# Optimization experiments

Hardware: AMD Instinct MI355X
Metric: run time of the kernel (lower is better)

## Reference

```python
import jax, jax.numpy as jnp
import numpy as np

P, V, D = 1024, 49408, 512


def setup_inputs() -> dict:
    key = jax.random.key(0)
    k1, k2 = jax.random.split(key)
    prompt_embs = jax.random.normal(k1, (P, D), dtype=jnp.float32)
    clip_embs = jax.random.normal(k2, (V, D), dtype=jnp.float32)
    return {"prompt_embs": prompt_embs, "clip_embs": clip_embs}


def reference(prompt_embs, clip_embs):
    # torch.cdist(p=2): Euclidean distance matrix [P, V].
    # ||a-b||^2 = ||a||^2 + ||b||^2 - 2 a.b ; sqrt is monotone so argmin of
    # the (clamped) squared distance matches argmin of the true distance.
    a2 = jnp.sum(prompt_embs * prompt_embs, axis=-1, keepdims=True)   # [P,1]
    b2 = jnp.sum(clip_embs * clip_embs, axis=-1)                      # [V]
    ab = jnp.einsum("pd,vd->pv", prompt_embs, clip_embs)              # [P,V]
    d2 = jnp.maximum(a2 + b2[None, :] - 2.0 * ab, 0.0)                # [P,V]
    prompt_ids = jnp.argmin(d2, axis=1)                               # [P]
    new_embs = clip_embs[prompt_ids]                                  # [P,D] gather
    return new_embs, prompt_ids
```

## Files before the change

### kernel.cpp

```cpp
#include <hip/hip_runtime.h>
#include <stdint.h>

#define NP 1024
#define NV 49408
#define ND 512
#define NTILE 48

typedef __attribute__((ext_vector_type(8))) __bf16 bf16x8;
typedef __attribute__((ext_vector_type(4))) float f32x4;
typedef __attribute__((ext_vector_type(4))) int i32x4;

__device__ inline unsigned long long pack_sv(float s, unsigned v) {
  unsigned u = __float_as_uint(s);
  u = (u & 0x80000000u) ? ~u : (u | 0x80000000u);
  return ((unsigned long long)u << 32) | (unsigned long long)v;
}

__global__ __launch_bounds__(256) void pack_a_k(const float* __restrict__ src,
                                                __bf16* __restrict__ dst) {
  int lane = threadIdx.x & 63;
  int row = blockIdx.x * 4 + (threadIdx.x >> 6);
  const float* r = src + (size_t)row * ND + lane * 8;
  float4 x0 = *(const float4*)r;
  float4 x1 = *(const float4*)(r + 4);
  float xs[8] = {x0.x, x0.y, x0.z, x0.w, x1.x, x1.y, x1.z, x1.w};
  bf16x8 hi, lo;
#pragma unroll
  for (int j = 0; j < 8; ++j) {
    float x = xs[j];
    __bf16 h = (__bf16)x;
    hi[j] = h;
    lo[j] = (__bf16)(x - (float)h);
  }
  const int mb = row >> 4, rr = row & 15;
  const int tHi = lane >> 2, g = lane & 3;
  size_t cHi = (((size_t)tHi * 64) + mb) * 64 + g * 16 + rr;
  size_t cLo = (((size_t)(tHi + 16) * 64) + mb) * 64 + g * 16 + rr;
  *(bf16x8*)(dst + cHi * 8) = hi;
  *(bf16x8*)(dst + cLo * 8) = lo;
}

__global__ __launch_bounds__(256) void pack_b_k(const float* __restrict__ src,
                                                __bf16* __restrict__ dst,
                                                float* __restrict__ sumsq) {
  int lane = threadIdx.x & 63;
  int row = blockIdx.x * 4 + (threadIdx.x >> 6);
  const float* r = src + (size_t)row * ND + lane * 8;
  float4 x0 = *(const float4*)r;
  float4 x1 = *(const float4*)(r + 4);
  float xs[8] = {x0.x, x0.y, x0.z, x0.w, x1.x, x1.y, x1.z, x1.w};
  bf16x8 hi, lo;
  float ss = 0.f;
#pragma unroll
  for (int j = 0; j < 8; ++j) {
    float x = xs[j];
    ss += x * x;
    __bf16 h = (__bf16)x;
    hi[j] = h;
    lo[j] = (__bf16)(x - (float)h);
  }
  __bf16* drow = dst + (size_t)row * 1024 + lane * 8;
  *(bf16x8*)drow = hi;
  *(bf16x8*)(drow + 512) = lo;
#pragma unroll
  for (int m = 1; m < 64; m <<= 1) ss += __shfl_xor(ss, m);
  if (lane == 0) sumsq[row] = ss;
}


__device__ __attribute__((always_inline)) static inline
void gll16(const char* src, char* dst) {
  __builtin_amdgcn_global_load_lds(
      (const __attribute__((address_space(1))) void*)src,
      (__attribute__((address_space(3))) void*)dst, 16, 0, 0);
}

__device__ __attribute__((always_inline)) static inline
bf16x8 lds_read(unsigned addr) {
  i32x4 d;
  asm volatile("ds_read_b128 %0, %1" : "=v"(d) : "v"(addr));
  return __builtin_bit_cast(bf16x8, d);
}

#define FENCE asm volatile("" ::: "memory")

template <int PH>
__device__ __attribute__((always_inline)) static inline
void phase_op(f32x4 (&acc)[4][4], bf16x8 (&aE)[4], bf16x8 (&aO)[4],
              const char* Ab, const int (&voffA)[4],
              const char* srcBt, char* stB, unsigned bRead, int p) {
  constexpr int R = PH % 3;
  constexpr int RS = (PH + 2) % 3;
  const int kA = ((p + 1) & 31) * 65536;
  const int t2 = p + 2;
  const int kB = (t2 & 15) * 64 + (t2 >= 32 ? 1024 : 0);
  bf16x8 (&aN)[4] = (PH % 2 == 0) ? aO : aE;
  bf16x8 (&aC)[4] = (PH % 2 == 0) ? aE : aO;
#pragma unroll
  for (int m = 0; m < 4; ++m)
    aN[m] = *(const bf16x8*)(Ab + voffA[m] + kA);
  gll16(srcBt + kB, stB + RS * 8192);
  gll16(srcBt + kB + 131072, stB + RS * 8192 + 4096);
  bf16x8 b[4];
#pragma unroll
  for (int n = 0; n < 4; ++n)
    b[n] = lds_read(bRead + R * 8192 + n * 1024);
  asm volatile("s_waitcnt vmcnt(6) lgkmcnt(0)" ::: "memory");
  __builtin_amdgcn_sched_barrier(0);
  __builtin_amdgcn_s_setprio(1);
#pragma unroll
  for (int m = 0; m < 4; ++m)
#pragma unroll
    for (int n = 0; n < 4; ++n)
      acc[m][n] = __builtin_amdgcn_mfma_f32_16x16x32_bf16(aC[m], b[n], acc[m][n], 0, 0, 0);
  __builtin_amdgcn_s_setprio(0);
  FENCE;
  __builtin_amdgcn_s_barrier();
  FENCE;
}

__global__ __launch_bounds__(256, 3) void gemm_argmin_k(const __bf16* __restrict__ A,
                                                        const __bf16* __restrict__ B,
                                                        const float* __restrict__ b2,
                                                        unsigned long long* __restrict__ best) {
  __shared__ __align__(16) char lds[24576];
  const int tid = threadIdx.x;
  const int lane = tid & 63;
  const int wid = tid >> 6;
  const int wm = wid >> 1;
  const int wn = wid & 1;

  const int d = blockIdx.x;
  const int o = (d & 7) * 386 + (d >> 3);
  const int bm = (o & 7) * 128;
  const int bn = (o >> 3) * 128;

  const int r = lane & 15, g = lane >> 4;
  const int rh = r >> 1;
  const unsigned lds0 =
      (unsigned)(uintptr_t)(const __attribute__((address_space(3))) char*)(const char*)lds;
  const unsigned bRead = lds0 + wn * 4096 + rh * 128 + (r & 1) * 64 + (((g + rh) & 3) << 4);

  const char* Ab = (const char*)A;
  int voffA[4];
#pragma unroll
  for (int m = 0; m < 4; ++m)
    voffA[m] = ((bm >> 4) + wm * 4 + m) * 1024 + lane * 16;

  const int srow = 2 * (tid >> 3) + ((tid >> 2) & 1);
  const int sc16 = ((tid & 3) - (tid >> 3)) & 3;
  const char* srcBt = (const char*)B + (size_t)(bn + srow) * 2048 + sc16 * 16;
  char* stB = (char*)lds + tid * 16;

  f32x4 acc[4][4] = {};
  bf16x8 aE[4], aO[4];

#pragma unroll
  for (int m = 0; m < 4; ++m)
    aE[m] = *(const bf16x8*)(Ab + voffA[m]);
  gll16(srcBt + 0, stB + 0);
  gll16(srcBt + 0 + 131072, stB + 4096);
  gll16(srcBt + 64, stB + 8192);
  gll16(srcBt + 64 + 131072, stB + 8192 + 4096);
  asm volatile("s_waitcnt vmcnt(2)" ::: "memory");
  FENCE;
  __builtin_amdgcn_s_barrier();
  FENCE;

#pragma unroll 1
  for (int it = 0; it < 8; ++it) {
    const int p0 = 6 * it;
    phase_op<0>(acc, aE, aO, Ab, voffA, srcBt, stB, bRead, p0 + 0);
    phase_op<1>(acc, aE, aO, Ab, voffA, srcBt, stB, bRead, p0 + 1);
    phase_op<2>(acc, aE, aO, Ab, voffA, srcBt, stB, bRead, p0 + 2);
    phase_op<3>(acc, aE, aO, Ab, voffA, srcBt, stB, bRead, p0 + 3);
    phase_op<4>(acc, aE, aO, Ab, voffA, srcBt, stB, bRead, p0 + 4);
    phase_op<5>(acc, aE, aO, Ab, voffA, srcBt, stB, bRead, p0 + 5);
  }

  float bb[4];
#pragma unroll
  for (int n = 0; n < 4; ++n) bb[n] = b2[bn + wn * 64 + n * 16 + r];
#pragma unroll
  for (int m = 0; m < 4; ++m) {
#pragma unroll
    for (int reg = 0; reg < 4; ++reg) {
      unsigned long long pk = ~0ull;
#pragma unroll
      for (int n = 0; n < 4; ++n) {
        float s = bb[n] - 2.0f * acc[m][n][reg];
        unsigned long long cand = pack_sv(s, (unsigned)(bn + wn * 64 + n * 16 + r));
        pk = (cand < pk) ? cand : pk;
      }
#pragma unroll
      for (int msk = 1; msk < 16; msk <<= 1) {
        unsigned long long o2 = __shfl_xor(pk, msk);
        pk = (o2 < pk) ? o2 : pk;
      }
      if (r == 0) atomicMin(&best[bm + wm * 64 + m * 16 + g * 4 + reg], pk);
    }
  }
}

__global__ __launch_bounds__(256) void naive_argmin_k(const float* __restrict__ A,
                                                      const float* __restrict__ B,
                                                      unsigned long long* __restrict__ best) {
  __shared__ float arow[ND];
  int p = blockIdx.y;
  unsigned v = blockIdx.x * 256 + threadIdx.x;
  for (int i = threadIdx.x; i < ND; i += 256) arow[i] = A[(size_t)p * ND + i];
  __syncthreads();
  const float4* br = (const float4*)(B + (size_t)v * ND);
  float s = 0.f;
#pragma unroll 4
  for (int i = 0; i < ND / 4; ++i) {
    float4 b = br[i];
    const float4 a = *(const float4*)&arow[i * 4];
    float d0 = a.x - b.x, d1 = a.y - b.y, d2 = a.z - b.z, d3 = a.w - b.w;
    s += d0 * d0 + d1 * d1 + d2 * d2 + d3 * d3;
  }
  unsigned long long pk = pack_sv(s, v);
#pragma unroll
  for (int msk = 1; msk < 64; msk <<= 1) {
    unsigned long long o = __shfl_xor(pk, msk);
    pk = (o < pk) ? o : pk;
  }
  if ((threadIdx.x & 63) == 0) atomicMin(&best[p], pk);
}

__global__ __launch_bounds__(128) void gather_k(const unsigned long long* __restrict__ best,
                                                const float* __restrict__ clip,
                                                float* __restrict__ out) {
  int p = blockIdx.x;
  unsigned long long pk = best[p];
  unsigned v = (unsigned)(pk & 0xffffffffull);
  const float4* src = (const float4*)(clip + (size_t)v * ND);
  float4* dst = (float4*)(out + (size_t)p * ND);
  dst[threadIdx.x] = src[threadIdx.x];
  if (threadIdx.x == 0) out[(size_t)NP * ND + p] = (float)v;
}

extern "C" void kernel_launch(void* const* d_in, const int* in_sizes, int n_in,
                              void* d_out, int out_size, void* d_ws, size_t ws_size,
                              hipStream_t stream) {
  const float* prompt = (const float*)d_in[0];
  const float* clip = (const float*)d_in[1];
  float* out = (float*)d_out;

  size_t off = 0;
  unsigned long long* best = (unsigned long long*)d_ws;
  off += (size_t)NP * 8;
  float* b2 = (float*)((char*)d_ws + off);
  off += (size_t)NV * 4;
  off = (off + 255) & ~(size_t)255;
  __bf16* Ap = (__bf16*)((char*)d_ws + off);
  off += (size_t)NP * 1024 * 2;
  __bf16* Bp = (__bf16*)((char*)d_ws + off);
  off += (size_t)NV * 1024 * 2;
  const size_t need = off;

  if (ws_size >= need) {
    hipMemsetAsync(best, 0xFF, (size_t)NP * 8, stream);
    pack_a_k<<<NP / 4, 256, 0, stream>>>(prompt, Ap);
    pack_b_k<<<NV / 4, 256, 0, stream>>>(clip, Bp, b2);
    gemm_argmin_k<<<dim3(8 * 386), 256, 0, stream>>>(Ap, Bp, b2, best);
    gather_k<<<NP, 128, 0, stream>>>(best, clip, out);
  } else {
    hipMemsetAsync(best, 0xFF, (size_t)NP * 8, stream);
    dim3 grid(NV / 256, NP);
    naive_argmin_k<<<grid, 256, 0, stream>>>(prompt, clip, best);
    gather_k<<<NP, 128, 0, stream>>>(best, clip, out);
  }
}
```

Before: 225.5 us.

## Deepen B LDS ring to four stages and prefetch B fragments into registers

The B-tile staging ring goes from three to four LDS stages, so global loads are issued three tiles ahead. B fragments are now double-buffered in registers: each phase reads the next tile's fragments from LDS while the MFMAs consume the current ones, and the wait is relaxed to lgkmcnt(4). The intent is to hide LDS read latency and global-load latency behind the matrix math. The cost is more LDS per block (32 KB), which may reduce occupancy under launch_bounds(256,3), and more vector registers.

```diff
diff --git a/kernel.cpp b/kernel.cpp
--- a/kernel.cpp
+++ b/kernel.cpp
@@ -84,35 +84,42 @@
 
 #define FENCE asm volatile("" ::: "memory")
 
-template <int PH>
+__device__ __attribute__((always_inline)) static inline
+int bByte(int t) {
+  int tt = (t < NTILE) ? t : t - NTILE;
+  return (tt & 15) * 64 + (tt >= 32 ? 1024 : 0);
+}
+
+template <int J>
 __device__ __attribute__((always_inline)) static inline
 void phase_op(f32x4 (&acc)[4][4], bf16x8 (&aE)[4], bf16x8 (&aO)[4],
+              bf16x8 (&bE)[4], bf16x8 (&bO)[4],
               const char* Ab, const int (&voffA)[4],
               const char* srcBt, char* stB, unsigned bRead, int p) {
-  constexpr int R = PH % 3;
-  constexpr int RS = (PH + 2) % 3;
+  constexpr int RS = (J + 3) & 3;
+  constexpr int RR = (J + 1) & 3;
+  const int kB = bByte(p + 3);
   const int kA = ((p + 1) & 31) * 65536;
-  const int t2 = p + 2;
-  const int kB = (t2 & 15) * 64 + (t2 >= 32 ? 1024 : 0);
-  bf16x8 (&aN)[4] = (PH % 2 == 0) ? aO : aE;
-  bf16x8 (&aC)[4] = (PH % 2 == 0) ? aE : aO;
-#pragma unroll
-  for (int m = 0; m < 4; ++m)
-    aN[m] = *(const bf16x8*)(Ab + voffA[m] + kA);
+  bf16x8 (&aN)[4] = (J % 2 == 0) ? aO : aE;
+  bf16x8 (&aC)[4] = (J % 2 == 0) ? aE : aO;
+  bf16x8 (&bN)[4] = (J % 2 == 0) ? bO : bE;
+  bf16x8 (&bC)[4] = (J % 2 == 0) ? bE : bO;
   gll16(srcBt + kB, stB + RS * 8192);
   gll16(srcBt + kB + 131072, stB + RS * 8192 + 4096);
-  bf16x8 b[4];
+#pragma unroll
+  for (int m = 0; m < 4; ++m)
+    aN[m] = *(const bf16x8*)(Ab + voffA[m] + kA);
 #pragma unroll
   for (int n = 0; n < 4; ++n)
-    b[n] = lds_read(bRead + R * 8192 + n * 1024);
-  asm volatile("s_waitcnt vmcnt(6) lgkmcnt(0)" ::: "memory");
+    bN[n] = lds_read(bRead + RR * 8192 + n * 1024);
+  asm volatile("s_waitcnt vmcnt(6) lgkmcnt(4)" ::: "memory");
   __builtin_amdgcn_sched_barrier(0);
   __builtin_amdgcn_s_setprio(1);
 #pragma unroll
   for (int m = 0; m < 4; ++m)
 #pragma unroll
     for (int n = 0; n < 4; ++n)
-      acc[m][n] = __builtin_amdgcn_mfma_f32_16x16x32_bf16(aC[m], b[n], acc[m][n], 0, 0, 0);
+      acc[m][n] = __builtin_amdgcn_mfma_f32_16x16x32_bf16(aC[m], bC[n], acc[m][n], 0, 0, 0);
   __builtin_amdgcn_s_setprio(0);
   FENCE;
   __builtin_amdgcn_s_barrier();
@@ -123,7 +130,7 @@
                                                         const __bf16* __restrict__ B,
                                                         const float* __restrict__ b2,
                                                         unsigned long long* __restrict__ best) {
-  __shared__ __align__(16) char lds[24576];
+  __shared__ __align__(16) char lds[32768];
   const int tid = threadIdx.x;
   const int lane = tid & 63;
   const int wid = tid >> 6;
@@ -153,29 +160,32 @@
   char* stB = (char*)lds + tid * 16;
 
   f32x4 acc[4][4] = {};
-  bf16x8 aE[4], aO[4];
-
+  bf16x8 aE[4], aO[4], bE[4], bO[4];
+
+  gll16(srcBt + bByte(0), stB + 0);
+  gll16(srcBt + bByte(0) + 131072, stB + 4096);
+  gll16(srcBt + bByte(1), stB + 8192);
+  gll16(srcBt + bByte(1) + 131072, stB + 8192 + 4096);
+  gll16(srcBt + bByte(2), stB + 16384);
+  gll16(srcBt + bByte(2) + 131072, stB + 16384 + 4096);
 #pragma unroll
   for (int m = 0; m < 4; ++m)
     aE[m] = *(const bf16x8*)(Ab + voffA[m]);
-  gll16(srcBt + 0, stB + 0);
-  gll16(srcBt + 0 + 131072, stB + 4096);
-  gll16(srcBt + 64, stB + 8192);
-  gll16(srcBt + 64 + 131072, stB + 8192 + 4096);
-  asm volatile("s_waitcnt vmcnt(2)" ::: "memory");
+  asm volatile("s_waitcnt vmcnt(6)" ::: "memory");
   FENCE;
   __builtin_amdgcn_s_barrier();
   FENCE;
+#pragma unroll
+  for (int n = 0; n < 4; ++n)
+    bE[n] = lds_read(bRead + n * 1024);
 
 #pragma unroll 1
-  for (int it = 0; it < 8; ++it) {
-    const int p0 = 6 * it;
-    phase_op<0>(acc, aE, aO, Ab, voffA, srcBt, stB, bRead, p0 + 0);
-    phase_op<1>(acc, aE, aO, Ab, voffA, srcBt, stB, bRead, p0 + 1);
-    phase_op<2>(acc, aE, aO, Ab, voffA, srcBt, stB, bRead, p0 + 2);
-    phase_op<3>(acc, aE, aO, Ab, voffA, srcBt, stB, bRead, p0 + 3);
-    phase_op<4>(acc, aE, aO, Ab, voffA, srcBt, stB, bRead, p0 + 4);
-    phase_op<5>(acc, aE, aO, Ab, voffA, srcBt, stB, bRead, p0 + 5);
+  for (int it = 0; it < 12; ++it) {
+    const int p0 = 4 * it;
+    phase_op<0>(acc, aE, aO, bE, bO, Ab, voffA, srcBt, stB, bRead, p0 + 0);
+    phase_op<1>(acc, aE, aO, bE, bO, Ab, voffA, srcBt, stB, bRead, p0 + 1);
+    phase_op<2>(acc, aE, aO, bE, bO, Ab, voffA, srcBt, stB, bRead, p0 + 2);
+    phase_op<3>(acc, aE, aO, bE, bO, Ab, voffA, srcBt, stB, bRead, p0 + 3);
   }
 
   float bb[4];
```

Result: no change. 222.7 us (-1.2%).
